# Optimization experiments

Measured on AMD Instinct MI355X. Metric: run time of the kernel, lower is better.

## Reference

```python
import jax, jax.numpy as jnp
import numpy as np

B, C4, N, L4 = 8, 64, 512, 12
CQ = C4 // 4  # conv output channels


def setup_inputs() -> dict:
    key = jax.random.key(0)
    k_x, k_wc, k_bc, k_wg, k_bg = jax.random.split(key, 5)
    x = jax.random.normal(k_x, (B, C4, N, L4), dtype=jnp.float32)
    # Conv2d(in_dim, in_dim//4, kernel_size=(1,1)) -> pointwise: weight (CQ, C4)
    W_conv = jax.random.normal(k_wc, (CQ, C4), dtype=jnp.float32) / np.sqrt(C4)
    b_conv = jax.random.normal(k_bc, (CQ,), dtype=jnp.float32) * 0.01
    # Linear(in_dim, in_dim)
    W_gcn = jax.random.normal(k_wg, (C4, C4), dtype=jnp.float32) / np.sqrt(C4)
    b_gcn = jax.random.normal(k_bg, (C4,), dtype=jnp.float32) * 0.01
    return {"x": x, "W_conv": W_conv, "b_conv": b_conv, "W_gcn": W_gcn, "b_gcn": b_gcn}


def reference(x, W_conv, b_conv, W_gcn, b_gcn):
    # --- SpatioTemporalCorrelationComputation ---
    # 1x1 conv over channels: (b,c4,n,l) -> (b,cq,n,l)
    Fc = jnp.einsum('oc,bcnl->bonl', W_conv, x) + b_conv[None, :, None, None]
    Fl = Fc[:, :, :, -1]                                   # b,cq,n (last time step)
    xy = jnp.einsum('bcn,bcmt->bnmt', Fl, Fc)              # b,n,n,l4
    xx = jnp.sqrt(jnp.einsum('bcn,bcn->bc', Fl, Fl))       # b,cq
    yy = jnp.sqrt(jnp.einsum('bcnt,bcnt->bc', Fc, Fc))     # b,cq
    l2 = jnp.einsum('bc,bc->b', xx, yy)[:, None, None, None]
    S = xy / l2                                            # b,n,n,l4

    # --- RelationalFeatureExtraction ---
    # Loop-based R[:, :, :, k] = sum_j S[:,k,None,:,j] * F4[:,:,:,j]
    # is exactly this single contraction (Se expansion never materialized):
    R = jnp.einsum('bknj,bcnj->bcnk', S, x)                # b,c4,n,n

    # --- GraphOperation ---
    A = jax.nn.relu(jnp.tanh(jnp.max(R, axis=1)))          # b,n,n
    xg = jnp.einsum('bcnk,bkn->bck', R, A)                 # b,c4,n
    # Linear over channel dim: Fg[b,o,k] = sum_c xg[b,c,k] W[o,c] + bias[o]
    Fg = jnp.einsum('bck,oc->bok', xg, W_gcn) + b_gcn[None, :, None]
    return Fg[..., None]                                   # b,c4,n,1
```

## Files before the change

### kernel.cpp

```cpp
#include <hip/hip_runtime.h>
#include <hip/hip_bf16.h>
#include <math.h>

#define B    8
#define C4   64
#define CQ   16
#define NN   512
#define L4   12
#define NCH1 8
#define KT   128

#define O_TH   0
#define O_TL   (O_TH + (size_t)B*1024*NN/2)
#define O_T2H  (O_TL + (size_t)B*1024*NN/2)
#define O_T2L  (O_T2H + (size_t)B*NN*1024/2)
#define O_FL   (O_T2L + (size_t)B*NN*1024/2)
#define O_FLTH (O_FL + (size_t)B*CQ*NN)
#define O_FLTL (O_FLTH + (size_t)B*NN*16/2)
#define O_XX   (O_FLTL + (size_t)B*NN*16/2)
#define O_YY   (O_XX + B*CQ)
#define O_L2   (O_YY + B*CQ)
#define O_AH   (O_L2 + 16)
#define O_AL   (O_AH + (size_t)B*NN*NN/2)
#define O_XG   (O_AL + (size_t)B*NN*NN/2)

typedef __attribute__((ext_vector_type(8))) short short8;
typedef __attribute__((ext_vector_type(4))) float floatx4;
typedef __attribute__((ext_vector_type(16))) float floatx16;

__device__ inline void split2(float x0, float x1, uint& hw, uint& lw) {
  uint u0 = __float_as_uint(x0), u1 = __float_as_uint(x1);
  uint h0 = u0 >> 16, h1 = u1 >> 16;
  float r0 = x0 - __uint_as_float(h0 << 16);
  float r1 = x1 - __uint_as_float(h1 << 16);
  hw = h0 | (h1 << 16);
  lw = (__float_as_uint(r0) >> 16) | ((__float_as_uint(r1) >> 16) << 16);
}

__global__ __launch_bounds__(256) void k1_fc(const float* __restrict__ x,
                                             const float* __restrict__ Wc,
                                             const float* __restrict__ bc,
                                             float* __restrict__ ws) {
  int blk = blockIdx.x;
  int b = blk >> 6;
  int n0 = (blk & 63) * NCH1;
  int t = threadIdx.x;
  __shared__ __align__(16) float xs[C4*NCH1*L4];
  __shared__ float wcs[CQ*C4];
  __shared__ float bcs[CQ];
  __shared__ __align__(16) float fcs[NCH1*CQ*L4];

  for (int e = t; e < CQ*C4; e += 256) wcs[e] = Wc[e];
  if (t < CQ) bcs[t] = bc[t];
  const float* xb = x + (size_t)b*C4*NN*L4 + (size_t)n0*L4;
  for (int f = t; f < (C4*NCH1*L4)/4; f += 256) {
    int c = f / (NCH1*L4/4);
    int r = f - c*(NCH1*L4/4);
    float4 v = *(const float4*)(xb + (size_t)c*NN*L4 + r*4);
    *(float4*)(xs + c*(NCH1*L4) + r*4) = v;
  }
  __syncthreads();
  for (int e = t; e < NCH1*CQ*L4; e += 256) {
    int nl = e / (CQ*L4);
    int rem = e - nl*(CQ*L4);
    int q = rem / L4, j = rem - q*L4;
    float acc = bcs[q];
    #pragma unroll
    for (int c = 0; c < C4; ++c) acc += wcs[q*C4 + c] * xs[c*(NCH1*L4) + nl*L4 + j];
    fcs[e] = acc;
    if (j == L4-1) ws[O_FL + ((size_t)b*CQ + q)*NN + n0 + nl] = acc;
  }
  __syncthreads();
  if (t < CQ) {
    float yy = 0.f, xx = 0.f;
    for (int nl = 0; nl < NCH1; ++nl) {
      #pragma unroll
      for (int j = 0; j < L4; ++j) { float v = fcs[nl*(CQ*L4) + t*L4 + j]; yy += v*v; }
      float w = fcs[nl*(CQ*L4) + t*L4 + (L4-1)];
      xx += w*w;
    }
    atomicAdd(ws + O_YY + b*CQ + t, yy);
    atomicAdd(ws + O_XX + b*CQ + t, xx);
  }
  {
    int c = t >> 2, q0 = (t & 3) * 4;
    float vals[4][NCH1];
    ushort* T2H = (ushort*)(ws + O_T2H);
    ushort* T2L = (ushort*)(ws + O_T2L);
    for (int nl = 0; nl < NCH1; ++nl) {
      float xr[L4];
      *(float4*)&xr[0] = *(const float4*)(xs + c*(NCH1*L4) + nl*L4);
      *(float4*)&xr[4] = *(const float4*)(xs + c*(NCH1*L4) + nl*L4 + 4);
      *(float4*)&xr[8] = *(const float4*)(xs + c*(NCH1*L4) + nl*L4 + 8);
      float tvp[4];
      #pragma unroll
      for (int i = 0; i < 4; ++i) {
        float a = 0.f;
        #pragma unroll
        for (int j = 0; j < L4; ++j) a += fcs[nl*(CQ*L4) + (q0+i)*L4 + j] * xr[j];
        tvp[i] = a;
        vals[i][nl] = a;
      }
      uint hw0, lw0, hw1, lw1;
      split2(tvp[0], tvp[1], hw0, lw0);
      split2(tvp[2], tvp[3], hw1, lw1);
      size_t off2 = ((size_t)b*NN + n0 + nl)*1024 + t*4;
      *(uint2*)(T2H + off2) = make_uint2(hw0, hw1);
      *(uint2*)(T2L + off2) = make_uint2(lw0, lw1);
    }
    ushort* TH = (ushort*)(ws + O_TH);
    ushort* TL = (ushort*)(ws + O_TL);
    #pragma unroll
    for (int i = 0; i < 4; ++i) {
      int m = c*16 + q0 + i;
      uint hw[4], lw[4];
      #pragma unroll
      for (int jj = 0; jj < 4; ++jj)
        split2(vals[i][2*jj], vals[i][2*jj+1], hw[jj], lw[jj]);
      size_t off = ((size_t)b*1024 + m)*NN + n0;
      *(uint4*)(TH + off) = make_uint4(hw[0], hw[1], hw[2], hw[3]);
      *(uint4*)(TL + off) = make_uint4(lw[0], lw[1], lw[2], lw[3]);
    }
  }
}

__global__ void k1b_l2(float* __restrict__ ws) {
  int t = threadIdx.x;
  __shared__ float s[B*CQ];
  s[t] = sqrtf(ws[O_XX + t]) * sqrtf(ws[O_YY + t]);
  __syncthreads();
  if (t < B) {
    float sum = 0.f;
    #pragma unroll
    for (int q = 0; q < CQ; ++q) sum += s[t*CQ + q];
    ws[O_L2 + t] = 1.0f / sum;
  }
}

__global__ __launch_bounds__(256) void k1c_flt(float* __restrict__ ws) {
  int idx = blockIdx.x*256 + threadIdx.x;
  int b = idx >> 9, k = idx & 511;
  const float* fl = ws + O_FL + (size_t)b*CQ*NN + k;
  ushort h[16], l[16];
  #pragma unroll
  for (int q = 0; q < CQ; ++q) {
    float v = fl[(size_t)q*NN];
    uint u = __float_as_uint(v);
    uint hh = u >> 16;
    float r = v - __uint_as_float(hh << 16);
    h[q] = (ushort)hh;
    l[q] = (ushort)(__float_as_uint(r) >> 16);
  }
  ushort* FH  = (ushort*)(ws + O_FLTH) + (size_t)idx*16;
  ushort* FLo = (ushort*)(ws + O_FLTL) + (size_t)idx*16;
  *(uint4*)(FH)      = *(uint4*)&h[0];
  *(uint4*)(FH + 8)  = *(uint4*)&h[8];
  *(uint4*)(FLo)     = *(uint4*)&l[0];
  *(uint4*)(FLo + 8) = *(uint4*)&l[8];
}

__global__ __launch_bounds__(256, 4) void k2_mfma(float* __restrict__ ws) {
  int id = blockIdx.x;
  int kh = id & 1;
  int nch = (id >> 1) & 63;
  int b = id >> 7;
  int t = threadIdx.x;
  int w = t >> 6, lane = t & 63;
  int col = lane & 31, half = lane >> 5;
  float l2inv = ws[O_L2 + b];
  const ushort* FltH = (const ushort*)(ws + O_FLTH);
  const ushort* FltL = (const ushort*)(ws + O_FLTL);
  short8 bhf[2], blf[2];
  int kcol[2];
  #pragma unroll
  for (int kt = 0; kt < 2; ++kt) {
    kcol[kt] = kh*256 + w*64 + kt*32 + col;
    size_t off = ((size_t)(b*NN + kcol[kt]))*16 + half*8;
    bhf[kt] = *(const short8*)(FltH + off);
    blf[kt] = *(const short8*)(FltL + off);
  }
  const ushort* T2H = (const ushort*)(ws + O_T2H) + ((size_t)b*NN + nch*8)*1024;
  const ushort* T2L = (const ushort*)(ws + O_T2L) + ((size_t)b*NN + nch*8)*1024;
  ushort* AH = (ushort*)(ws + O_AH) + ((size_t)b*NN + nch*8)*NN;
  ushort* AL = (ushort*)(ws + O_AL) + ((size_t)b*NN + nch*8)*NN;

  for (int i = 0; i < 8; ++i) {
    short8 ah[2], al[2];
    #pragma unroll
    for (int ct = 0; ct < 2; ++ct) {
      size_t off = (size_t)i*1024 + (ct*32 + col)*16 + half*8;
      ah[ct] = *(const short8*)(T2H + off);
      al[ct] = *(const short8*)(T2L + off);
    }
    floatx16 acc[2][2];
    #pragma unroll
    for (int ct = 0; ct < 2; ++ct)
      #pragma unroll
      for (int kt = 0; kt < 2; ++kt) {
        floatx16 a = {0.f,0.f,0.f,0.f,0.f,0.f,0.f,0.f,
                      0.f,0.f,0.f,0.f,0.f,0.f,0.f,0.f};
        a = __builtin_amdgcn_mfma_f32_32x32x16_bf16(ah[ct], bhf[kt], a, 0, 0, 0);
        a = __builtin_amdgcn_mfma_f32_32x32x16_bf16(ah[ct], blf[kt], a, 0, 0, 0);
        a = __builtin_amdgcn_mfma_f32_32x32x16_bf16(al[ct], bhf[kt], a, 0, 0, 0);
        acc[ct][kt] = a;
      }
    #pragma unroll
    for (int kt = 0; kt < 2; ++kt) {
      float m = acc[0][kt][0];
      #pragma unroll
      for (int ct = 0; ct < 2; ++ct)
        #pragma unroll
        for (int rg = 0; rg < 16; ++rg)
          if (ct + rg) m = fmaxf(m, acc[ct][kt][rg]);
      m = fmaxf(m, __shfl_xor(m, 32));
      float av = fmaxf(tanhf(m*l2inv), 0.f);
      uint u = __float_as_uint(av);
      uint hh = u >> 16;
      float r = av - __uint_as_float(hh << 16);
      ushort lv = (ushort)(__float_as_uint(r) >> 16);
      if (half == 0) {
        AH[(size_t)i*NN + kcol[kt]] = (ushort)hh;
        AL[(size_t)i*NN + kcol[kt]] = lv;
      }
    }
  }
}

__global__ __launch_bounds__(256, 2) void k3_mfma(float* __restrict__ ws) {
  int id = blockIdx.x;
  int kb = id & 7;
  int mbb = (id >> 3) & 7;
  int b = id >> 6;
  int t = threadIdx.x;
  int lane = t & 63;
  int w = t >> 6;
  int mw = w >> 1, kw = w & 1;
  int row = lane & 15, quad = lane >> 4;

  __shared__ __align__(16) ushort Ah[128*32];
  __shared__ __align__(16) ushort Al[128*32];
  __shared__ __align__(16) ushort Bh[64*32];
  __shared__ __align__(16) ushort Bl[64*32];

  const ushort* TH = (const ushort*)(ws + O_TH) + ((size_t)b*1024 + mbb*128)*NN;
  const ushort* TL = (const ushort*)(ws + O_TL) + ((size_t)b*1024 + mbb*128)*NN;
  const ushort* AHp = (const ushort*)(ws + O_AH) + ((size_t)b*NN + kb*64)*NN;
  const ushort* ALp = (const ushort*)(ws + O_AL) + ((size_t)b*NN + kb*64)*NN;

  floatx4 acc[4][2];
  #pragma unroll
  for (int i = 0; i < 4; ++i)
    #pragma unroll
    for (int j = 0; j < 2; ++j) acc[i][j] = (floatx4){0.f, 0.f, 0.f, 0.f};

  for (int ksx = 0; ksx < 16; ++ksx) {
    int p0 = ksx*32;
    __syncthreads();
    #pragma unroll
    for (int i = 0; i < 2; ++i) {
      int f = t + 256*i;
      int m = f >> 2, seg = (f & 3) * 8;
      *(uint4*)(Ah + m*32 + seg) = *(const uint4*)(TH + (size_t)m*NN + p0 + seg);
      *(uint4*)(Al + m*32 + seg) = *(const uint4*)(TL + (size_t)m*NN + p0 + seg);
    }
    {
      int j = t >> 2, seg = (t & 3) * 8;
      *(uint4*)(Bh + j*32 + seg) = *(const uint4*)(AHp + (size_t)j*NN + p0 + seg);
      *(uint4*)(Bl + j*32 + seg) = *(const uint4*)(ALp + (size_t)j*NN + p0 + seg);
    }
    __syncthreads();
    short8 bh[2], bl[2];
    #pragma unroll
    for (int kt = 0; kt < 2; ++kt) {
      int jrow = kw*32 + kt*16 + row;
      bh[kt] = *(const short8*)(Bh + jrow*32 + quad*8);
      bl[kt] = *(const short8*)(Bl + jrow*32 + quad*8);
    }
    #pragma unroll
    for (int mt = 0; mt < 4; ++mt) {
      int mrow = mw*64 + mt*16 + row;
      short8 ah = *(const short8*)(Ah + mrow*32 + quad*8);
      short8 al = *(const short8*)(Al + mrow*32 + quad*8);
      #pragma unroll
      for (int kt = 0; kt < 2; ++kt) {
        acc[mt][kt] = __builtin_amdgcn_mfma_f32_16x16x32_bf16(ah, bh[kt], acc[mt][kt], 0, 0, 0);
        acc[mt][kt] = __builtin_amdgcn_mfma_f32_16x16x32_bf16(ah, bl[kt], acc[mt][kt], 0, 0, 0);
        acc[mt][kt] = __builtin_amdgcn_mfma_f32_16x16x32_bf16(al, bh[kt], acc[mt][kt], 0, 0, 0);
      }
    }
  }
  float l2inv = ws[O_L2 + b];
  const float* flb = ws + O_FL + (size_t)b*CQ*NN;
  float fl[2][4];
  #pragma unroll
  for (int kt = 0; kt < 2; ++kt) {
    int kcol = kb*64 + kw*32 + kt*16 + row;
    #pragma unroll
    for (int rg = 0; rg < 4; ++rg)
      fl[kt][rg] = flb[(size_t)(quad*4 + rg)*NN + kcol];
  }
  #pragma unroll
  for (int mt = 0; mt < 4; ++mt) {
    int c = mbb*8 + mw*4 + mt;
    #pragma unroll
    for (int kt = 0; kt < 2; ++kt) {
      float s = fl[kt][0]*acc[mt][kt][0] + fl[kt][1]*acc[mt][kt][1]
              + fl[kt][2]*acc[mt][kt][2] + fl[kt][3]*acc[mt][kt][3];
      s += __shfl_xor(s, 32);
      s += __shfl_xor(s, 16);
      if (quad == 0) {
        int kcol = kb*64 + kw*32 + kt*16 + row;
        ws[O_XG + ((size_t)b*C4 + c)*NN + kcol] = s * l2inv;
      }
    }
  }
}

__global__ __launch_bounds__(256) void k4_out(const float* __restrict__ Wg,
                                              const float* __restrict__ bg,
                                              const float* __restrict__ ws,
                                              float* __restrict__ out) {
  int blk = blockIdx.x;
  int b = blk >> 2, kc = blk & 3;
  int t = threadIdx.x;
  __shared__ float xg[C4][KT+1];
  __shared__ float wg[C4*C4];
  for (int e = t; e < C4*C4; e += 256) wg[e] = Wg[e];
  for (int e = t; e < C4*KT; e += 256) {
    int c = e >> 7, kk = e & (KT-1);
    xg[c][kk] = ws[O_XG + ((size_t)(b*C4 + c))*NN + kc*KT + kk];
  }
  __syncthreads();
  int kk = t & (KT-1);
  int ohalf = t >> 7;
  for (int oi = 0; oi < 32; ++oi) {
    int o = ohalf*32 + oi;
    float acc = bg[o];
    #pragma unroll
    for (int c = 0; c < C4; ++c) acc += wg[o*C4 + c] * xg[c][kk];
    out[((size_t)(b*C4 + o))*NN + kc*KT + kk] = acc;
  }
}

extern "C" void kernel_launch(void* const* d_in, const int* in_sizes, int n_in,
                              void* d_out, int out_size, void* d_ws, size_t ws_size,
                              hipStream_t stream) {
  const float* x  = (const float*)d_in[0];
  const float* Wc = (const float*)d_in[1];
  const float* bc = (const float*)d_in[2];
  const float* Wg = (const float*)d_in[3];
  const float* bg = (const float*)d_in[4];
  float* ws  = (float*)d_ws;
  float* out = (float*)d_out;

  hipMemsetAsync(ws + O_XX, 0, (2*B*CQ + 16)*sizeof(float), stream);

  k1_fc   <<<B*64,   256, 0, stream>>>(x, Wc, bc, ws);
  k1b_l2  <<<1,      128, 0, stream>>>(ws);
  k1c_flt <<<16,     256, 0, stream>>>(ws);
  k2_mfma <<<B*128,  256, 0, stream>>>(ws);
  k3_mfma <<<B*64,   256, 0, stream>>>(ws);
  k4_out  <<<B*4,    256, 0, stream>>>(Wg, bg, ws, out);
}
```

Baseline: 163.3 us.

## Split k3 reduction into two halves and register-block k1 conv

k3_mfma now splits the 512-long p reduction across two blocks, doubling the grid to B*128 and raising the launch-bounds occupancy hint to 4. Each half writes a partial xg buffer, and k4_out sums the two partials when it loads them. k1_fc is also reworked: each thread accumulates 6 outputs with one weight load per channel, and the weight smem rows are padded to 65 to avoid bank conflicts. The aim is better GPU fill in k3 and less redundant smem traffic in k1, at the cost of extra partial-buffer writes and reads.

```diff
diff --git a/kernel.cpp b/kernel.cpp
--- a/kernel.cpp
+++ b/kernel.cpp
@@ -22,7 +22,7 @@
 #define O_L2   (O_YY + B*CQ)
 #define O_AH   (O_L2 + 16)
 #define O_AL   (O_AH + (size_t)B*NN*NN/2)
-#define O_XG   (O_AL + (size_t)B*NN*NN/2)
+#define O_XGP  (O_AL + (size_t)B*NN*NN/2)
 
 typedef __attribute__((ext_vector_type(8))) short short8;
 typedef __attribute__((ext_vector_type(4))) float floatx4;
@@ -46,11 +46,14 @@
   int n0 = (blk & 63) * NCH1;
   int t = threadIdx.x;
   __shared__ __align__(16) float xs[C4*NCH1*L4];
-  __shared__ float wcs[CQ*C4];
+  __shared__ float wcs[CQ*65];
   __shared__ float bcs[CQ];
   __shared__ __align__(16) float fcs[NCH1*CQ*L4];
 
-  for (int e = t; e < CQ*C4; e += 256) wcs[e] = Wc[e];
+  for (int e = t; e < CQ*C4; e += 256) {
+    int q = e >> 6, c = e & 63;
+    wcs[q*65 + c] = Wc[e];
+  }
   if (t < CQ) bcs[t] = bc[t];
   const float* xb = x + (size_t)b*C4*NN*L4 + (size_t)n0*L4;
   for (int f = t; f < (C4*NCH1*L4)/4; f += 256) {
@@ -60,15 +63,24 @@
     *(float4*)(xs + c*(NCH1*L4) + r*4) = v;
   }
   __syncthreads();
-  for (int e = t; e < NCH1*CQ*L4; e += 256) {
-    int nl = e / (CQ*L4);
-    int rem = e - nl*(CQ*L4);
-    int q = rem / L4, j = rem - q*L4;
-    float acc = bcs[q];
-    #pragma unroll
-    for (int c = 0; c < C4; ++c) acc += wcs[q*C4 + c] * xs[c*(NCH1*L4) + nl*L4 + j];
-    fcs[e] = acc;
-    if (j == L4-1) ws[O_FL + ((size_t)b*CQ + q)*NN + n0 + nl] = acc;
+  {
+    int q = t & 15, slot = t >> 4;
+    float accv[6];
+    #pragma unroll
+    for (int i = 0; i < 6; ++i) accv[i] = bcs[q];
+    for (int c = 0; c < C4; ++c) {
+      float wv = wcs[q*65 + c];
+      const float* xc = xs + c*(NCH1*L4);
+      #pragma unroll
+      for (int i = 0; i < 6; ++i) accv[i] += wv * xc[slot + 16*i];
+    }
+    #pragma unroll
+    for (int i = 0; i < 6; ++i) {
+      int nj = slot + 16*i;
+      int nl = nj / L4, j = nj - nl*L4;
+      fcs[nl*(CQ*L4) + q*L4 + j] = accv[i];
+      if (j == L4-1) ws[O_FL + ((size_t)b*CQ + q)*NN + n0 + nl] = accv[i];
+    }
   }
   __syncthreads();
   if (t < CQ) {
@@ -226,11 +238,12 @@
   }
 }
 
-__global__ __launch_bounds__(256, 2) void k3_mfma(float* __restrict__ ws) {
+__global__ __launch_bounds__(256, 4) void k3_mfma(float* __restrict__ ws) {
   int id = blockIdx.x;
   int kb = id & 7;
   int mbb = (id >> 3) & 7;
-  int b = id >> 6;
+  int ns = (id >> 6) & 1;
+  int b = id >> 7;
   int t = threadIdx.x;
   int lane = t & 63;
   int w = t >> 6;
@@ -253,8 +266,8 @@
     #pragma unroll
     for (int j = 0; j < 2; ++j) acc[i][j] = (floatx4){0.f, 0.f, 0.f, 0.f};
 
-  for (int ksx = 0; ksx < 16; ++ksx) {
-    int p0 = ksx*32;
+  for (int ksx = 0; ksx < 8; ++ksx) {
+    int p0 = ns*256 + ksx*32;
     __syncthreads();
     #pragma unroll
     for (int i = 0; i < 2; ++i) {
@@ -310,7 +323,7 @@
       s += __shfl_xor(s, 16);
       if (quad == 0) {
         int kcol = kb*64 + kw*32 + kt*16 + row;
-        ws[O_XG + ((size_t)b*C4 + c)*NN + kcol] = s * l2inv;
+        ws[O_XGP + (((size_t)(b*2 + ns)*C4 + c)*NN) + kcol] = s * l2inv;
       }
     }
   }
@@ -328,7 +341,8 @@
   for (int e = t; e < C4*C4; e += 256) wg[e] = Wg[e];
   for (int e = t; e < C4*KT; e += 256) {
     int c = e >> 7, kk = e & (KT-1);
-    xg[c][kk] = ws[O_XG + ((size_t)(b*C4 + c))*NN + kc*KT + kk];
+    xg[c][kk] = ws[O_XGP + (((size_t)(b*2 + 0)*C4 + c)*NN) + kc*KT + kk]
+              + ws[O_XGP + (((size_t)(b*2 + 1)*C4 + c)*NN) + kc*KT + kk];
   }
   __syncthreads();
   int kk = t & (KT-1);
@@ -359,6 +373,6 @@
   k1b_l2  <<<1,      128, 0, stream>>>(ws);
   k1c_flt <<<16,     256, 0, stream>>>(ws);
   k2_mfma <<<B*128,  256, 0, stream>>>(ws);
-  k3_mfma <<<B*64,   256, 0, stream>>>(ws);
+  k3_mfma <<<B*128,  256, 0, stream>>>(ws);
   k4_out  <<<B*4,    256, 0, stream>>>(Wg, bg, ws, out);
 }
```

Measured after the change: 165.3 us. Within noise of the previous version (+1.2%).
